# Performance work log

Hardware: AMD Instinct MI355X
Metric: run time of the kernel (lower is better)

Reference implementation:

```python
import jax, jax.numpy as jnp
import numpy as np

N_TOKEN = 267735
CUTOFFS = [20000, 40000, 200000, N_TOKEN]  # includes final n_token
D_EMBED = 1024
D_PROJ = 1024
DIV_VAL = 4
N = 1024  # number of tokens


def setup_inputs() -> dict:
    key = jax.random.key(0)
    ks = jax.random.split(key, 20)
    inp = {}
    inp['hidden'] = jax.random.normal(ks[0], (N, D_PROJ), dtype=jnp.float32)
    inp['target'] = jax.random.randint(ks[1], (N,), 0, N_TOKEN, dtype=jnp.int64)
    cutoff_ends = [0] + CUTOFFS
    # per-cluster params: weight [vocab_i, d_emb_i], bias [vocab_i], proj [d_proj, d_emb_i]
    for i in range(4):
        l, r = cutoff_ends[i], cutoff_ends[i + 1]
        d_i = D_EMBED // (DIV_VAL ** i)
        s = 1.0 / np.sqrt(d_i)
        inp[f'W{i}'] = jax.random.uniform(ks[2 + 3 * i], (r - l, d_i), minval=-s, maxval=s, dtype=jnp.float32)
        inp[f'b{i}'] = jnp.zeros((r - l,), dtype=jnp.float32)
        inp[f'proj{i}'] = jax.random.uniform(ks[3 + 3 * i], (D_PROJ, d_i), minval=-s, maxval=s, dtype=jnp.float32)
    inp['cluster_W'] = jax.random.normal(ks[15], (3, D_EMBED), dtype=jnp.float32) * 0.02
    inp['cluster_b'] = jnp.zeros((3,), dtype=jnp.float32)
    return inp


def _adaptive_nll(hidden, target, W0, b0, proj0, W1, b1, proj1, W2, b2, proj2, W3, b3, proj3, cluster_W, cluster_b):
    cutoff_ends = [0] + CUTOFFS
    # head: shortlist vocab + 3 cluster logits
    head_w = jnp.concatenate([W0, cluster_W], axis=0)          # [20003, d_embed]
    head_b = jnp.concatenate([b0, cluster_b], axis=0)          # [20003]
    head_logit = (hidden @ proj0) @ head_w.T + head_b          # [N, 20003]
    head_lp = jax.nn.log_softmax(head_logit, axis=1)
    # shortlist cluster (i == 0)
    t0 = jnp.clip(target, 0, cutoff_ends[1] - 1)
    lp0 = jnp.take_along_axis(head_lp, t0[:, None], axis=1)[:, 0]
    m0 = target < cutoff_ends[1]
    nll = jnp.where(m0, -lp0, 0.0)
    # tail clusters; faithful to original: head column is head_lp[:, -i]
    tails = [(W1, b1, proj1), (W2, b2, proj2), (W3, b3, proj3)]
    for i, (W_i, b_i, proj_i) in enumerate(tails, start=1):
        l, r = cutoff_ends[i], cutoff_ends[i + 1]
        tail_logit = (hidden @ proj_i) @ W_i.T + b_i           # [N, r-l]
        tail_lp = jax.nn.log_softmax(tail_logit, axis=1)
        ti = jnp.clip(target - l, 0, r - l - 1)
        lp_tail = jnp.take_along_axis(tail_lp, ti[:, None], axis=1)[:, 0]
        lp_i = head_lp[:, -i] + lp_tail
        m_i = (target >= l) & (target < r)
        nll = nll + jnp.where(m_i, -lp_i, 0.0)
    return nll.mean()  # reduction='mean'


def reference(hidden, target, W0, b0, proj0, W1, b1, proj1, W2, b2, proj2, W3, b3, proj3, cluster_W, cluster_b):
    return _adaptive_nll(hidden, target, W0, b0, proj0, W1, b1, proj1, W2, b2, proj2, W3, b3, proj3, cluster_W, cluster_b)
```

## Files before the change

### kernel.cpp

```cpp
#include <hip/hip_runtime.h>
#include <stdint.h>


typedef __attribute__((ext_vector_type(8))) short short8;
typedef __attribute__((ext_vector_type(4))) float f32x4;

__device__ __forceinline__ float bf2f(unsigned short u) {
    union { unsigned int i; float f; } v; v.i = ((unsigned int)u) << 16; return v.f;
}
__device__ __forceinline__ unsigned short f2bf(float f) {
    union { float f; unsigned int i; } v; v.f = f;
    unsigned int u = v.i;
    return (unsigned short)((u + 0x7fffu + ((u >> 16) & 1u)) >> 16);
}
__device__ __forceinline__ float wave_sum(float v) {
    v += __shfl_xor(v, 1, 64);  v += __shfl_xor(v, 2, 64);
    v += __shfl_xor(v, 4, 64);  v += __shfl_xor(v, 8, 64);
    v += __shfl_xor(v, 16, 64); v += __shfl_xor(v, 32, 64);
    return v;
}
__device__ __forceinline__ short8 pack8(float4 a, float4 b) {
    union { int4 i; short8 s; } r;
    r.i.x = __builtin_amdgcn_perm(__float_as_uint(a.y), __float_as_uint(a.x), 0x07060302u);
    r.i.y = __builtin_amdgcn_perm(__float_as_uint(a.w), __float_as_uint(a.z), 0x07060302u);
    r.i.z = __builtin_amdgcn_perm(__float_as_uint(b.y), __float_as_uint(b.x), 0x07060302u);
    r.i.w = __builtin_amdgcn_perm(__float_as_uint(b.w), __float_as_uint(b.z), 0x07060302u);
    return r.s;
}

template <int NK32, int KD>
__device__ __forceinline__ void dev_convw(int bid, const float* __restrict__ W,
                                          unsigned short* __restrict__ Wf,
                                          int vocab, int units) {
    int u = bid * 4 + (threadIdx.x >> 6);
    if (u >= units) return;
    int lane = threadIdx.x & 63, q = lane >> 4, ln = lane & 15;
    int row = u * 16 + ln;
    bool rv = row < vocab;
    const float* src = W + (size_t)row * KD;
#pragma unroll
    for (int ks = 0; ks < NK32; ++ks) {
        int k0 = ks * 32 + q * 8;
        float4 a = {0.f, 0.f, 0.f, 0.f}, b = {0.f, 0.f, 0.f, 0.f};
        if (rv && k0 < KD) {
            a = *(const float4*)(src + k0);
            b = *(const float4*)(src + k0 + 4);
        }
        *(short8*)(Wf + ((size_t)u * NK32 + ks) * 512 + lane * 8) = pack8(a, b);
    }
}

__device__ __forceinline__ void dev_transpose(int bx, int by,
                                              const float* __restrict__ src,
                                              unsigned short* __restrict__ dst,
                                              int K, int N) {
    __shared__ unsigned short tile[32][33];
    int k0 = by * 32, n0 = bx * 32;
    int tx = threadIdx.x & 31, ty = threadIdx.x >> 5;
#pragma unroll
    for (int j = 0; j < 4; ++j) {
        int k = k0 + ty + j * 8, n = n0 + tx;
        float v = (n < N) ? src[(size_t)k * N + n] : 0.f;
        tile[ty + j * 8][tx] = f2bf(v);
    }
    __syncthreads();
#pragma unroll
    for (int j = 0; j < 4; ++j) {
        int n = n0 + ty + j * 8, k = k0 + tx;
        if (n < N) dst[(size_t)n * K + k] = tile[tx][ty + j * 8];
    }
}

__global__ __launch_bounds__(256)
void k_prep(const float* __restrict__ hidden, unsigned short* __restrict__ hid_bf,
            const float* __restrict__ W0, unsigned short* __restrict__ W0f,
            const float* __restrict__ W1, unsigned short* __restrict__ W1f,
            const float* __restrict__ W2, unsigned short* __restrict__ W2f,
            const float* __restrict__ W3, unsigned short* __restrict__ W3f,
            const float* __restrict__ proj0, unsigned short* __restrict__ pT0,
            const float* __restrict__ proj1, unsigned short* __restrict__ pT1,
            const float* __restrict__ proj2, unsigned short* __restrict__ pT2,
            const float* __restrict__ proj3, unsigned short* __restrict__ pT3) {
    int bid = blockIdx.x, tid = threadIdx.x;
    if (bid < 1024) {
        int i = bid * 256 + tid;
        float4 v = ((const float4*)hidden)[i];
        ushort4 o;
        o.x = f2bf(v.x); o.y = f2bf(v.y); o.z = f2bf(v.z); o.w = f2bf(v.w);
        ((ushort4*)hid_bf)[i] = o;
    }
    else if (bid < 1337) dev_convw<32, 1024>(bid - 1024, W0, W0f, 20000, 1250);
    else if (bid < 1650) dev_convw<8,  256> (bid - 1337, W1, W1f, 20000, 1250);
    else if (bid < 4150) dev_convw<2,  64>  (bid - 1650, W2, W2f, 160000, 10000);
    else if (bid < 5209) dev_convw<1,  16>  (bid - 4150, W3, W3f, 67735, 4234);
    else if (bid < 6233) { int i = bid - 5209; dev_transpose(i & 31, i >> 5, proj0, pT0, 1024, 1024); }
    else if (bid < 6489) { int i = bid - 6233; dev_transpose(i & 7,  i >> 3, proj1, pT1, 1024, 256); }
    else if (bid < 6553) { int i = bid - 6489; dev_transpose(i & 1,  i >> 1, proj2, pT2, 1024, 64); }
    else                 { int i = bid - 6553; dev_transpose(0,      i,      proj3, pT3, 1024, 16); }
}

#define BM 128
#define BN 128
#define BK 64
#define LDT 72
template <int NK32O>
__device__ __forceinline__ void dev_gemm(unsigned short* __restrict__ ls,
                                         int bx, int by,
                                         const unsigned short* __restrict__ A, int lda,
                                         const unsigned short* __restrict__ B, int ldb,
                                         unsigned short* __restrict__ Cf,
                                         int N, int K) {
    unsigned short* lsA = ls;
    unsigned short* lsB = ls + BM * LDT;
    int tid = threadIdx.x;
    int mBase = bx * BM, nBase = by * BN;
    int wid = tid >> 6, lane = tid & 63;
    int wr = wid >> 1, wc = wid & 1;
    int q = lane >> 4, ln = lane & 15;
    f32x4 acc[4][4] = {};

    for (int k0 = 0; k0 < K; k0 += BK) {
        __syncthreads();
        int ch = tid & 7;
#pragma unroll
        for (int p = 0; p < 4; ++p) {
            int r = p * 32 + (tid >> 3);
            *(uint4*)(&lsA[r * LDT + ch * 8]) =
                *(const uint4*)(A + (size_t)(mBase + r) * lda + k0 + ch * 8);
        }
#pragma unroll
        for (int p = 0; p < 4; ++p) {
            int r = p * 32 + (tid >> 3);
            uint4 v = {0u, 0u, 0u, 0u};
            if (nBase + r < N)
                v = *(const uint4*)(B + (size_t)(nBase + r) * ldb + k0 + ch * 8);
            *(uint4*)(&lsB[r * LDT + ch * 8]) = v;
        }
        __syncthreads();
#pragma unroll
        for (int ks = 0; ks < 2; ++ks) {
            short8 af[4], bfr[4];
#pragma unroll
            for (int mi = 0; mi < 4; ++mi)
                af[mi] = *(const short8*)(&lsA[(wr * 64 + mi * 16 + ln) * LDT + ks * 32 + q * 8]);
#pragma unroll
            for (int ni = 0; ni < 4; ++ni)
                bfr[ni] = *(const short8*)(&lsB[(wc * 64 + ni * 16 + ln) * LDT + ks * 32 + q * 8]);
#pragma unroll
            for (int mi = 0; mi < 4; ++mi)
#pragma unroll
                for (int ni = 0; ni < 4; ++ni)
                    acc[mi][ni] = __builtin_amdgcn_mfma_f32_16x16x32_bf16(
                        af[mi], bfr[ni], acc[mi][ni], 0, 0, 0);
        }
    }
#pragma unroll
    for (int ni = 0; ni < 4; ++ni) {
        int col = nBase + wc * 64 + ni * 16 + ln;
        if (col < N) {
            int k32 = col >> 5, qc = (col >> 3) & 3, j = col & 7;
#pragma unroll
            for (int mi = 0; mi < 4; ++mi) {
                int m16 = (mBase >> 4) + wr * 4 + mi;
                size_t base = ((size_t)m16 * NK32O + k32) * 512 + (size_t)qc * 128 + j;
#pragma unroll
                for (int r = 0; r < 4; ++r) {
                    int mrem = q * 4 + r;
                    Cf[base + mrem * 8] = f2bf(acc[mi][ni][r]);
                }
            }
        }
    }
}

__global__ __launch_bounds__(256)
void k_gemm_all(const unsigned short* __restrict__ hid_bf,
                const unsigned short* __restrict__ pT0, const unsigned short* __restrict__ pT1,
                const unsigned short* __restrict__ pT2, const unsigned short* __restrict__ pT3,
                unsigned short* __restrict__ h0f, unsigned short* __restrict__ h1f,
                unsigned short* __restrict__ h2f, unsigned short* __restrict__ h3f) {
    __shared__ unsigned short ls[(BM + BN) * LDT];
    int bid = blockIdx.x;
    if (bid < 64)      dev_gemm<32>(ls, bid & 7, bid >> 3, hid_bf, 1024, pT0, 1024, h0f, 1024, 1024);
    else if (bid < 80) { int i = bid - 64; dev_gemm<8>(ls, i & 7, i >> 3, hid_bf, 1024, pT1, 1024, h1f, 256, 1024); }
    else if (bid < 88) dev_gemm<2>(ls, bid - 80, 0, hid_bf, 1024, pT2, 1024, h2f, 64, 1024);
    else               dev_gemm<1>(ls, bid - 88, 0, hid_bf, 1024, pT3, 1024, h3f, 16, 1024);
}

__device__ __forceinline__ void dev_head(int f,
                const unsigned short* __restrict__ Af,
                const unsigned short* __restrict__ Wf,
                const float* __restrict__ bias,
                float* __restrict__ rowsum, int vocab) {
    int u = f & 63;
    int xb = u >> 3;
    int yb = ((f >> 6) << 3) + (u & 7);
    if (yb * 128 >= vocab) return;

    int tid = threadIdx.x, wid = tid >> 6, lane = tid & 63;
    int wr = wid >> 1, wc = wid & 1;
    int q = lane >> 4, ln = lane & 15;
    int mb = xb * 128 + wr * 64;
    int nb = yb * 128 + wc * 64;
    int units = (vocab + 15) >> 4;

    const unsigned short* Ab = Af + (size_t)(mb >> 4) * 32 * 512 + lane * 8;
    const unsigned short* Wp[4];
#pragma unroll
    for (int ni = 0; ni < 4; ++ni)
        Wp[ni] = Wf + (size_t)min((nb >> 4) + ni, units - 1) * 32 * 512 + lane * 8;

    f32x4 acc[4][4] = {};
    short8 Abf[3][4], Wbf[3][4];
    auto LA = [&](short8* d, int kk) {
#pragma unroll
        for (int mi = 0; mi < 4; ++mi)
            d[mi] = *(const short8*)(Ab + ((size_t)mi * 32 + kk) * 512);
    };
    auto LW = [&](short8* d, int kk) {
#pragma unroll
        for (int ni = 0; ni < 4; ++ni)
            d[ni] = *(const short8*)(Wp[ni] + (size_t)kk * 512);
    };
    auto FM = [&](short8* a, short8* w) {
#pragma unroll
        for (int mi = 0; mi < 4; ++mi)
#pragma unroll
            for (int ni = 0; ni < 4; ++ni)
                acc[mi][ni] = __builtin_amdgcn_mfma_f32_16x16x32_bf16(
                    a[mi], w[ni], acc[mi][ni], 0, 0, 0);
    };

    LA(Abf[0], 0); LW(Wbf[0], 0);
    LA(Abf[1], 1); LW(Wbf[1], 1);
#pragma unroll
    for (int ks = 0; ks < 32; ++ks) {
        int nxt = (ks + 2) % 3, cur = ks % 3;
        if (ks + 2 < 32) { LA(Abf[nxt], ks + 2); LW(Wbf[nxt], ks + 2); }
        FM(Abf[cur], Wbf[cur]);
    }

    float s[4][4];
#pragma unroll
    for (int mi = 0; mi < 4; ++mi)
#pragma unroll
        for (int r = 0; r < 4; ++r) s[mi][r] = 0.f;
#pragma unroll
    for (int ni = 0; ni < 4; ++ni) {
        int col = nb + ni * 16 + ln;
        bool valid = col < vocab;
        float b = valid ? bias[col] : 0.f;
#pragma unroll
        for (int mi = 0; mi < 4; ++mi)
#pragma unroll
            for (int r = 0; r < 4; ++r)
                s[mi][r] += valid ? __expf(acc[mi][ni][r] + b) : 0.f;
    }
#pragma unroll
    for (int mi = 0; mi < 4; ++mi)
#pragma unroll
        for (int r = 0; r < 4; ++r) {
            float v = s[mi][r];
            v += __shfl_xor(v, 1, 64);
            v += __shfl_xor(v, 2, 64);
            v += __shfl_xor(v, 4, 64);
            v += __shfl_xor(v, 8, 64);
            s[mi][r] = v;
        }
    int sl = yb & 31;
    if (ln == 0) {
#pragma unroll
        for (int mi = 0; mi < 4; ++mi)
#pragma unroll
            for (int r = 0; r < 4; ++r)
                atomicAdd(&rowsum[sl * 1024 + mb + mi * 16 + q * 4 + r], s[mi][r]);
    }
}

template <int NK32>
__device__ __forceinline__ void dev_tail(int bx, int by,
                const unsigned short* __restrict__ Af,
                const unsigned short* __restrict__ Wf,
                const float* __restrict__ bias,
                float* __restrict__ rowsum,
                int vocab, int units, int ngroups) {
    int tid = threadIdx.x;
    int wid = tid >> 6, lane = tid & 63;
    int q = lane >> 4, ln = lane & 15;
    int m16b = by * 16 + wid * 4;
    int u0 = bx * ngroups;

    short8 af[4][NK32];
#pragma unroll
    for (int mi = 0; mi < 4; ++mi)
#pragma unroll
        for (int ks = 0; ks < NK32; ++ks)
            af[mi][ks] = *(const short8*)(Af + ((size_t)(m16b + mi) * NK32 + ks) * 512 + lane * 8);

    float rs[4][4];
#pragma unroll
    for (int mi = 0; mi < 4; ++mi)
#pragma unroll
        for (int r = 0; r < 4; ++r) rs[mi][r] = 0.f;

    const unsigned short* Wb = Wf + (size_t)lane * 8;
    auto LWG = [&](short8* d, int u) {
        int uc = min(u, units - 1);
#pragma unroll
        for (int ks = 0; ks < NK32; ++ks)
            d[ks] = *(const short8*)(Wb + ((size_t)uc * NK32 + ks) * 512);
    };
    auto CG = [&](short8* w, int u) {
        f32x4 acc[4] = {};
#pragma unroll
        for (int ks = 0; ks < NK32; ++ks)
#pragma unroll
            for (int mi = 0; mi < 4; ++mi)
                acc[mi] = __builtin_amdgcn_mfma_f32_16x16x32_bf16(
                    af[mi][ks], w[ks], acc[mi], 0, 0, 0);
        int col = u * 16 + ln;
        bool valid = col < vocab;
        float b = valid ? bias[col] : 0.f;
#pragma unroll
        for (int mi = 0; mi < 4; ++mi)
#pragma unroll
            for (int r = 0; r < 4; ++r)
                rs[mi][r] += valid ? __expf(acc[mi][r] + b) : 0.f;
    };

    short8 w0[NK32], w1[NK32];
    LWG(w0, u0);
    int g = 0;
    for (; g + 1 < ngroups; g += 2) {
        LWG(w1, u0 + g + 1);
        CG(w0, u0 + g);
        LWG(w0, u0 + g + 2);
        CG(w1, u0 + g + 1);
    }
    if (g < ngroups) CG(w0, u0 + g);

    int sl = bx & 31;
#pragma unroll
    for (int mi = 0; mi < 4; ++mi)
#pragma unroll
        for (int r = 0; r < 4; ++r) {
            float v = rs[mi][r];
            v += __shfl_xor(v, 1, 64);
            v += __shfl_xor(v, 2, 64);
            v += __shfl_xor(v, 4, 64);
            v += __shfl_xor(v, 8, 64);
            if (ln == 0)
                atomicAdd(&rowsum[sl * 1024 + (m16b + mi) * 16 + q * 4 + r], v);
        }
}

__device__ __forceinline__ float frag_dot(const unsigned short* __restrict__ hf,
                                          int NK32, int KdReal, int n,
                                          const float* __restrict__ wrow, int lane) {
    float s = 0.f;
    for (int c = lane; c * 8 < KdReal; c += 64) {
        int k32 = c >> 2, qq = c & 3;
        const unsigned short* p = hf + ((size_t)(n >> 4) * NK32 + k32) * 512 + (qq * 16 + (n & 15)) * 8;
#pragma unroll
        for (int j = 0; j < 8; ++j)
            s += bf2f(p[j]) * wrow[c * 8 + j];
    }
    return wave_sum(s);
}

__device__ __forceinline__ void dev_gather(int bid,
                         const unsigned short* __restrict__ h0f,
                         const unsigned short* __restrict__ h1f,
                         const unsigned short* __restrict__ h2f,
                         const unsigned short* __restrict__ h3f,
                         const float* __restrict__ W0, const float* __restrict__ b0,
                         const float* __restrict__ W1, const float* __restrict__ b1,
                         const float* __restrict__ W2, const float* __restrict__ b2,
                         const float* __restrict__ W3, const float* __restrict__ b3,
                         const float* __restrict__ cW, const float* __restrict__ cb,
                         const int* __restrict__ target,
                         float* __restrict__ rowsum0,
                         float* __restrict__ gat_head,
                         float* __restrict__ gat_tail) {
    int gw = bid * 4 + (threadIdx.x >> 6);
    int lane = threadIdx.x & 63;
    if (gw >= 1024) return;
    int n = gw;
    int t = target[n];

    float cl[3];
#pragma unroll
    for (int j = 0; j < 3; ++j)
        cl[j] = frag_dot(h0f, 32, 1024, n, cW + j * 1024, lane) + cb[j];
    if (lane == 0)
        atomicAdd(&rowsum0[n], __expf(cl[0]) + __expf(cl[1]) + __expf(cl[2]));

    float gh, gt = 0.f;
    if (t < 20000) {
        gh = frag_dot(h0f, 32, 1024, n, W0 + (size_t)t * 1024, lane) + b0[t];
    } else {
        int c, l, Kd, NK32;
        const unsigned short* h; const float* W; const float* b;
        if (t < 40000)       { c = 1; l = 20000;  Kd = 256; NK32 = 8; h = h1f; W = W1; b = b1; }
        else if (t < 200000) { c = 2; l = 40000;  Kd = 64;  NK32 = 2; h = h2f; W = W2; b = b2; }
        else                 { c = 3; l = 200000; Kd = 16;  NK32 = 1; h = h3f; W = W3; b = b3; }
        gh = cl[3 - c];
        gt = frag_dot(h, NK32, Kd, n, W + (size_t)(t - l) * Kd, lane) + b[t - l];
    }
    if (lane == 0) { gat_head[n] = gh; gat_tail[n] = gt; }
}

__global__ __launch_bounds__(256, 2)
void k_logit_all(const unsigned short* __restrict__ h0f, const unsigned short* __restrict__ h1f,
                 const unsigned short* __restrict__ h2f, const unsigned short* __restrict__ h3f,
                 const unsigned short* __restrict__ W0f, const unsigned short* __restrict__ W1f,
                 const unsigned short* __restrict__ W2f, const unsigned short* __restrict__ W3f,
                 const float* __restrict__ W0, const float* __restrict__ b0,
                 const float* __restrict__ W1, const float* __restrict__ b1,
                 const float* __restrict__ W2, const float* __restrict__ b2,
                 const float* __restrict__ W3, const float* __restrict__ b3,
                 const float* __restrict__ cW, const float* __restrict__ cb,
                 const int* __restrict__ target,
                 float* __restrict__ rowsum,
                 float* __restrict__ gat_head, float* __restrict__ gat_tail) {
    int bid = blockIdx.x;
    if (bid < 1280) {
        dev_head(bid, h0f, W0f, b0, rowsum, 20000);
    } else if (bid < 1536) {
        int i = bid - 1280;
        dev_tail<8>(i & 63, i >> 6, h1f, W1f, b1, rowsum + 32768, 20000, 1250, 20);
    } else if (bid < 2176) {
        int i = bid - 1536;
        dev_tail<2>(i % 160, i / 160, h2f, W2f, b2, rowsum + 65536, 160000, 10000, 63);
    } else if (bid < 2688) {
        int i = bid - 2176;
        dev_tail<1>(i & 127, i >> 7, h3f, W3f, b3, rowsum + 98304, 67735, 4234, 34);
    } else {
        dev_gather(bid - 2688, h0f, h1f, h2f, h3f, W0, b0, W1, b1, W2, b2, W3, b3,
                   cW, cb, target, rowsum, gat_head, gat_tail);
    }
}

__global__ void k_finalize(const float* __restrict__ rs,
                           const float* __restrict__ gat_head,
                           const float* __restrict__ gat_tail,
                           const int* __restrict__ target,
                           float* __restrict__ out) {
    __shared__ float red[16];
    int n = threadIdx.x;
    int t = target[n];
    float r0 = 0.f;
#pragma unroll
    for (int s = 0; s < 32; ++s) r0 += rs[s * 1024 + n];
    float nll = __logf(r0) - gat_head[n];
    int c = (t < 20000) ? 0 : (t < 40000) ? 1 : (t < 200000) ? 2 : 3;
    if (c > 0) {
        float rc = 0.f;
#pragma unroll
        for (int s = 0; s < 32; ++s) rc += rs[c * 32768 + s * 1024 + n];
        nll += __logf(rc) - gat_tail[n];
    }
    float sm = wave_sum(nll);
    int wid = n >> 6, lane = n & 63;
    if (lane == 0) red[wid] = sm;
    __syncthreads();
    if (n == 0) {
        float tot = 0.f;
#pragma unroll
        for (int i = 0; i < 16; ++i) tot += red[i];
        out[0] = tot / 1024.0f;
    }
}

extern "C" void kernel_launch(void* const* d_in, const int* in_sizes, int n_in,
                              void* d_out, int out_size, void* d_ws, size_t ws_size,
                              hipStream_t stream) {
    const float* hidden = (const float*)d_in[0];
    const int*   target = (const int*)d_in[1];
    const float* W0 = (const float*)d_in[2];
    const float* b0 = (const float*)d_in[3];
    const float* proj0 = (const float*)d_in[4];
    const float* W1 = (const float*)d_in[5];
    const float* b1 = (const float*)d_in[6];
    const float* proj1 = (const float*)d_in[7];
    const float* W2 = (const float*)d_in[8];
    const float* b2 = (const float*)d_in[9];
    const float* proj2 = (const float*)d_in[10];
    const float* W3 = (const float*)d_in[11];
    const float* b3 = (const float*)d_in[12];
    const float* proj3 = (const float*)d_in[13];
    const float* cW = (const float*)d_in[14];
    const float* cb = (const float*)d_in[15];

    char* ws = (char*)d_ws;
    unsigned short* hid_bf = (unsigned short*)(ws + 0x000000);
    unsigned short* pT0 = (unsigned short*)(ws + 0x200000);
    unsigned short* pT1 = (unsigned short*)(ws + 0x400000);
    unsigned short* pT2 = (unsigned short*)(ws + 0x480000);
    unsigned short* pT3 = (unsigned short*)(ws + 0x4A0000);
    unsigned short* h0f = (unsigned short*)(ws + 0x4A8000);
    unsigned short* h1f = (unsigned short*)(ws + 0x6A8000);
    unsigned short* h2f = (unsigned short*)(ws + 0x728000);
    unsigned short* h3f = (unsigned short*)(ws + 0x748000);
    float* rowsum   = (float*)(ws + 0x758000);
    float* gat_head = (float*)(ws + 0x7D8000);
    float* gat_tail = (float*)(ws + 0x7D9000);
    unsigned short* W0f = (unsigned short*)(ws + 0x00800000);
    unsigned short* W1f = (unsigned short*)(ws + 0x02F10000);
    unsigned short* W2f = (unsigned short*)(ws + 0x038D4000);
    unsigned short* W3f = (unsigned short*)(ws + 0x04C5C000);

    hipMemsetAsync(ws + 0x748000, 0, 0x92000, stream);

    k_prep<<<6585, 256, 0, stream>>>(hidden, hid_bf, W0, W0f, W1, W1f, W2, W2f, W3, W3f,
                                     proj0, pT0, proj1, pT1, proj2, pT2, proj3, pT3);

    k_gemm_all<<<96, 256, 0, stream>>>(hid_bf, pT0, pT1, pT2, pT3, h0f, h1f, h2f, h3f);

    k_logit_all<<<2944, 256, 0, stream>>>(h0f, h1f, h2f, h3f, W0f, W1f, W2f, W3f,
                                          W0, b0, W1, b1, W2, b2, W3, b3,
                                          cW, cb, target, rowsum, gat_head, gat_tail);

    k_finalize<<<1, 1024, 0, stream>>>(rowsum, gat_head, gat_tail, target, (float*)d_out);
}
```

Measured before the change: 412.8 us.

## Overlap weight conversion with projection GEMMs and pad biases to drop bounds checks

Moves the large fp32-to-bf16 weight repacking out of the prep kernel and into the same launch as the projection GEMMs, so the few GEMM blocks run alongside the bandwidth-bound conversion. Biases are copied into padded buffers filled with -1e30 so the logit kernels can drop per-column validity checks and clamped unit indices. The head-style tiled streaming kernel is templated and reused for cluster 1 in place of the tail kernel, and its software pipeline uses two buffers instead of three. This adds extra workspace and a bias-fill pass, and changes how work is split across the GPU for the middle cluster.

```diff
diff --git a/kernel.cpp b/kernel.cpp
--- a/kernel.cpp
+++ b/kernel.cpp
@@ -28,28 +28,6 @@
     return r.s;
 }
 
-template <int NK32, int KD>
-__device__ __forceinline__ void dev_convw(int bid, const float* __restrict__ W,
-                                          unsigned short* __restrict__ Wf,
-                                          int vocab, int units) {
-    int u = bid * 4 + (threadIdx.x >> 6);
-    if (u >= units) return;
-    int lane = threadIdx.x & 63, q = lane >> 4, ln = lane & 15;
-    int row = u * 16 + ln;
-    bool rv = row < vocab;
-    const float* src = W + (size_t)row * KD;
-#pragma unroll
-    for (int ks = 0; ks < NK32; ++ks) {
-        int k0 = ks * 32 + q * 8;
-        float4 a = {0.f, 0.f, 0.f, 0.f}, b = {0.f, 0.f, 0.f, 0.f};
-        if (rv && k0 < KD) {
-            a = *(const float4*)(src + k0);
-            b = *(const float4*)(src + k0 + 4);
-        }
-        *(short8*)(Wf + ((size_t)u * NK32 + ks) * 512 + lane * 8) = pack8(a, b);
-    }
-}
-
 __device__ __forceinline__ void dev_transpose(int bx, int by,
                                               const float* __restrict__ src,
                                               unsigned short* __restrict__ dst,
@@ -71,16 +49,22 @@
     }
 }
 
+__device__ __forceinline__ void dev_biasfill(int bid, const float* __restrict__ b,
+                                             float* __restrict__ bp, int vocab, int padded) {
+    int i = bid * 256 + threadIdx.x;
+    if (i < padded) bp[i] = (i < vocab) ? b[i] : -1e30f;
+}
+
 __global__ __launch_bounds__(256)
-void k_prep(const float* __restrict__ hidden, unsigned short* __restrict__ hid_bf,
-            const float* __restrict__ W0, unsigned short* __restrict__ W0f,
-            const float* __restrict__ W1, unsigned short* __restrict__ W1f,
-            const float* __restrict__ W2, unsigned short* __restrict__ W2f,
-            const float* __restrict__ W3, unsigned short* __restrict__ W3f,
-            const float* __restrict__ proj0, unsigned short* __restrict__ pT0,
-            const float* __restrict__ proj1, unsigned short* __restrict__ pT1,
-            const float* __restrict__ proj2, unsigned short* __restrict__ pT2,
-            const float* __restrict__ proj3, unsigned short* __restrict__ pT3) {
+void k_pre(const float* __restrict__ hidden, unsigned short* __restrict__ hid_bf,
+           const float* __restrict__ proj0, unsigned short* __restrict__ pT0,
+           const float* __restrict__ proj1, unsigned short* __restrict__ pT1,
+           const float* __restrict__ proj2, unsigned short* __restrict__ pT2,
+           const float* __restrict__ proj3, unsigned short* __restrict__ pT3,
+           const float* __restrict__ b0, float* __restrict__ b0p,
+           const float* __restrict__ b1, float* __restrict__ b1p,
+           const float* __restrict__ b2, float* __restrict__ b2p,
+           const float* __restrict__ b3, float* __restrict__ b3p) {
     int bid = blockIdx.x, tid = threadIdx.x;
     if (bid < 1024) {
         int i = bid * 256 + tid;
@@ -89,14 +73,36 @@
         o.x = f2bf(v.x); o.y = f2bf(v.y); o.z = f2bf(v.z); o.w = f2bf(v.w);
         ((ushort4*)hid_bf)[i] = o;
     }
-    else if (bid < 1337) dev_convw<32, 1024>(bid - 1024, W0, W0f, 20000, 1250);
-    else if (bid < 1650) dev_convw<8,  256> (bid - 1337, W1, W1f, 20000, 1250);
-    else if (bid < 4150) dev_convw<2,  64>  (bid - 1650, W2, W2f, 160000, 10000);
-    else if (bid < 5209) dev_convw<1,  16>  (bid - 4150, W3, W3f, 67735, 4234);
-    else if (bid < 6233) { int i = bid - 5209; dev_transpose(i & 31, i >> 5, proj0, pT0, 1024, 1024); }
-    else if (bid < 6489) { int i = bid - 6233; dev_transpose(i & 7,  i >> 3, proj1, pT1, 1024, 256); }
-    else if (bid < 6553) { int i = bid - 6489; dev_transpose(i & 1,  i >> 1, proj2, pT2, 1024, 64); }
-    else                 { int i = bid - 6553; dev_transpose(0,      i,      proj3, pT3, 1024, 16); }
+    else if (bid < 2048) { int i = bid - 1024; dev_transpose(i & 31, i >> 5, proj0, pT0, 1024, 1024); }
+    else if (bid < 2304) { int i = bid - 2048; dev_transpose(i & 7,  i >> 3, proj1, pT1, 1024, 256); }
+    else if (bid < 2368) { int i = bid - 2304; dev_transpose(i & 1,  i >> 1, proj2, pT2, 1024, 64); }
+    else if (bid < 2400) { int i = bid - 2368; dev_transpose(0,      i,      proj3, pT3, 1024, 16); }
+    else if (bid < 2479) dev_biasfill(bid - 2400, b0, b0p, 20000, 20096);
+    else if (bid < 2558) dev_biasfill(bid - 2479, b1, b1p, 20000, 20096);
+    else if (bid < 3188) dev_biasfill(bid - 2558, b2, b2p, 160000, 161280);
+    else                 dev_biasfill(bid - 3188, b3, b3p, 67735, 69632);
+}
+
+template <int NK32, int KD>
+__device__ __forceinline__ void dev_convw(int bid, const float* __restrict__ W,
+                                          unsigned short* __restrict__ Wf,
+                                          int vocab, int upad) {
+    int u = bid * 4 + (threadIdx.x >> 6);
+    if (u >= upad) return;
+    int lane = threadIdx.x & 63, q = lane >> 4, ln = lane & 15;
+    int row = u * 16 + ln;
+    bool rv = row < vocab;
+    const float* src = W + (size_t)row * KD;
+#pragma unroll
+    for (int ks = 0; ks < NK32; ++ks) {
+        int k0 = ks * 32 + q * 8;
+        float4 a = {0.f, 0.f, 0.f, 0.f}, b = {0.f, 0.f, 0.f, 0.f};
+        if (rv && k0 < KD) {
+            a = *(const float4*)(src + k0);
+            b = *(const float4*)(src + k0 + 4);
+        }
+        *(short8*)(Wf + ((size_t)u * NK32 + ks) * 512 + lane * 8) = pack8(a, b);
+    }
 }
 
 #define BM 128
@@ -174,48 +180,56 @@
 }
 
 __global__ __launch_bounds__(256)
-void k_gemm_all(const unsigned short* __restrict__ hid_bf,
-                const unsigned short* __restrict__ pT0, const unsigned short* __restrict__ pT1,
-                const unsigned short* __restrict__ pT2, const unsigned short* __restrict__ pT3,
-                unsigned short* __restrict__ h0f, unsigned short* __restrict__ h1f,
-                unsigned short* __restrict__ h2f, unsigned short* __restrict__ h3f) {
+void k_mid(const unsigned short* __restrict__ hid_bf,
+           const unsigned short* __restrict__ pT0, const unsigned short* __restrict__ pT1,
+           const unsigned short* __restrict__ pT2, const unsigned short* __restrict__ pT3,
+           unsigned short* __restrict__ h0f, unsigned short* __restrict__ h1f,
+           unsigned short* __restrict__ h2f, unsigned short* __restrict__ h3f,
+           const float* __restrict__ W0, unsigned short* __restrict__ W0f,
+           const float* __restrict__ W1, unsigned short* __restrict__ W1f,
+           const float* __restrict__ W2, unsigned short* __restrict__ W2f,
+           const float* __restrict__ W3, unsigned short* __restrict__ W3f) {
     __shared__ unsigned short ls[(BM + BN) * LDT];
     int bid = blockIdx.x;
-    if (bid < 64)      dev_gemm<32>(ls, bid & 7, bid >> 3, hid_bf, 1024, pT0, 1024, h0f, 1024, 1024);
-    else if (bid < 80) { int i = bid - 64; dev_gemm<8>(ls, i & 7, i >> 3, hid_bf, 1024, pT1, 1024, h1f, 256, 1024); }
-    else if (bid < 88) dev_gemm<2>(ls, bid - 80, 0, hid_bf, 1024, pT2, 1024, h2f, 64, 1024);
-    else               dev_gemm<1>(ls, bid - 88, 0, hid_bf, 1024, pT3, 1024, h3f, 16, 1024);
-}
-
-__device__ __forceinline__ void dev_head(int f,
+    if (bid < 64)        dev_gemm<32>(ls, bid & 7, bid >> 3, hid_bf, 1024, pT0, 1024, h0f, 1024, 1024);
+    else if (bid < 80)   { int i = bid - 64; dev_gemm<8>(ls, i & 7, i >> 3, hid_bf, 1024, pT1, 1024, h1f, 256, 1024); }
+    else if (bid < 88)   dev_gemm<2>(ls, bid - 80, 0, hid_bf, 1024, pT2, 1024, h2f, 64, 1024);
+    else if (bid < 96)   dev_gemm<1>(ls, bid - 88, 0, hid_bf, 1024, pT3, 1024, h3f, 16, 1024);
+    else if (bid < 410)  dev_convw<32, 1024>(bid - 96,   W0, W0f, 20000, 1256);
+    else if (bid < 724)  dev_convw<8,  256> (bid - 410,  W1, W1f, 20000, 1256);
+    else if (bid < 3244) dev_convw<2,  64>  (bid - 724,  W2, W2f, 160000, 10080);
+    else                 dev_convw<1,  16>  (bid - 3244, W3, W3f, 67735, 4352);
+}
+
+template <int NK32>
+__device__ __forceinline__ void dev_stream(int f,
                 const unsigned short* __restrict__ Af,
                 const unsigned short* __restrict__ Wf,
-                const float* __restrict__ bias,
-                float* __restrict__ rowsum, int vocab) {
+                const float* __restrict__ biasp,
+                float* __restrict__ rowsum) {
     int u = f & 63;
     int xb = u >> 3;
     int yb = ((f >> 6) << 3) + (u & 7);
-    if (yb * 128 >= vocab) return;
+    if (yb >= 157) return;
 
     int tid = threadIdx.x, wid = tid >> 6, lane = tid & 63;
     int wr = wid >> 1, wc = wid & 1;
     int q = lane >> 4, ln = lane & 15;
     int mb = xb * 128 + wr * 64;
     int nb = yb * 128 + wc * 64;
-    int units = (vocab + 15) >> 4;
-
-    const unsigned short* Ab = Af + (size_t)(mb >> 4) * 32 * 512 + lane * 8;
+
+    const unsigned short* Ab = Af + (size_t)(mb >> 4) * NK32 * 512 + lane * 8;
     const unsigned short* Wp[4];
 #pragma unroll
     for (int ni = 0; ni < 4; ++ni)
-        Wp[ni] = Wf + (size_t)min((nb >> 4) + ni, units - 1) * 32 * 512 + lane * 8;
+        Wp[ni] = Wf + (size_t)((nb >> 4) + ni) * NK32 * 512 + lane * 8;
 
     f32x4 acc[4][4] = {};
-    short8 Abf[3][4], Wbf[3][4];
+    short8 a0[4], a1[4], w0[4], w1[4];
     auto LA = [&](short8* d, int kk) {
 #pragma unroll
         for (int mi = 0; mi < 4; ++mi)
-            d[mi] = *(const short8*)(Ab + ((size_t)mi * 32 + kk) * 512);
+            d[mi] = *(const short8*)(Ab + ((size_t)mi * NK32 + kk) * 512);
     };
     auto LW = [&](short8* d, int kk) {
 #pragma unroll
@@ -231,13 +245,13 @@
                     a[mi], w[ni], acc[mi][ni], 0, 0, 0);
     };
 
-    LA(Abf[0], 0); LW(Wbf[0], 0);
-    LA(Abf[1], 1); LW(Wbf[1], 1);
-#pragma unroll
-    for (int ks = 0; ks < 32; ++ks) {
-        int nxt = (ks + 2) % 3, cur = ks % 3;
-        if (ks + 2 < 32) { LA(Abf[nxt], ks + 2); LW(Wbf[nxt], ks + 2); }
-        FM(Abf[cur], Wbf[cur]);
+    LA(a0, 0); LW(w0, 0);
+#pragma unroll
+    for (int ks = 0; ks < NK32; ks += 2) {
+        LA(a1, ks + 1); LW(w1, ks + 1);
+        FM(a0, w0);
+        if (ks + 2 < NK32) { LA(a0, ks + 2); LW(w0, ks + 2); }
+        FM(a1, w1);
     }
 
     float s[4][4];
@@ -247,14 +261,12 @@
         for (int r = 0; r < 4; ++r) s[mi][r] = 0.f;
 #pragma unroll
     for (int ni = 0; ni < 4; ++ni) {
-        int col = nb + ni * 16 + ln;
-        bool valid = col < vocab;
-        float b = valid ? bias[col] : 0.f;
+        float b = biasp[nb + ni * 16 + ln];
 #pragma unroll
         for (int mi = 0; mi < 4; ++mi)
 #pragma unroll
             for (int r = 0; r < 4; ++r)
-                s[mi][r] += valid ? __expf(acc[mi][ni][r] + b) : 0.f;
+                s[mi][r] += __expf(acc[mi][ni][r] + b);
     }
 #pragma unroll
     for (int mi = 0; mi < 4; ++mi)
@@ -281,9 +293,8 @@
 __device__ __forceinline__ void dev_tail(int bx, int by,
                 const unsigned short* __restrict__ Af,
                 const unsigned short* __restrict__ Wf,
-                const float* __restrict__ bias,
-                float* __restrict__ rowsum,
-                int vocab, int units, int ngroups) {
+                const float* __restrict__ biasp,
+                float* __restrict__ rowsum, int ngroups) {
     int tid = threadIdx.x;
     int wid = tid >> 6, lane = tid & 63;
     int q = lane >> 4, ln = lane & 15;
@@ -305,10 +316,9 @@
 
     const unsigned short* Wb = Wf + (size_t)lane * 8;
     auto LWG = [&](short8* d, int u) {
-        int uc = min(u, units - 1);
 #pragma unroll
         for (int ks = 0; ks < NK32; ++ks)
-            d[ks] = *(const short8*)(Wb + ((size_t)uc * NK32 + ks) * 512);
+            d[ks] = *(const short8*)(Wb + ((size_t)u * NK32 + ks) * 512);
     };
     auto CG = [&](short8* w, int u) {
         f32x4 acc[4] = {};
@@ -318,14 +328,12 @@
             for (int mi = 0; mi < 4; ++mi)
                 acc[mi] = __builtin_amdgcn_mfma_f32_16x16x32_bf16(
                     af[mi][ks], w[ks], acc[mi], 0, 0, 0);
-        int col = u * 16 + ln;
-        bool valid = col < vocab;
-        float b = valid ? bias[col] : 0.f;
+        float b = biasp[u * 16 + ln];
 #pragma unroll
         for (int mi = 0; mi < 4; ++mi)
 #pragma unroll
             for (int r = 0; r < 4; ++r)
-                rs[mi][r] += valid ? __expf(acc[mi][r] + b) : 0.f;
+                rs[mi][r] += __expf(acc[mi][r] + b);
     };
 
     short8 w0[NK32], w1[NK32];
@@ -415,6 +423,8 @@
                  const unsigned short* __restrict__ h2f, const unsigned short* __restrict__ h3f,
                  const unsigned short* __restrict__ W0f, const unsigned short* __restrict__ W1f,
                  const unsigned short* __restrict__ W2f, const unsigned short* __restrict__ W3f,
+                 const float* __restrict__ b0p, const float* __restrict__ b1p,
+                 const float* __restrict__ b2p, const float* __restrict__ b3p,
                  const float* __restrict__ W0, const float* __restrict__ b0,
                  const float* __restrict__ W1, const float* __restrict__ b1,
                  const float* __restrict__ W2, const float* __restrict__ b2,
@@ -425,18 +435,17 @@
                  float* __restrict__ gat_head, float* __restrict__ gat_tail) {
     int bid = blockIdx.x;
     if (bid < 1280) {
-        dev_head(bid, h0f, W0f, b0, rowsum, 20000);
-    } else if (bid < 1536) {
-        int i = bid - 1280;
-        dev_tail<8>(i & 63, i >> 6, h1f, W1f, b1, rowsum + 32768, 20000, 1250, 20);
-    } else if (bid < 2176) {
-        int i = bid - 1536;
-        dev_tail<2>(i % 160, i / 160, h2f, W2f, b2, rowsum + 65536, 160000, 10000, 63);
-    } else if (bid < 2688) {
-        int i = bid - 2176;
-        dev_tail<1>(i & 127, i >> 7, h3f, W3f, b3, rowsum + 98304, 67735, 4234, 34);
+        dev_stream<32>(bid, h0f, W0f, b0p, rowsum);
+    } else if (bid < 2560) {
+        dev_stream<8>(bid - 1280, h1f, W1f, b1p, rowsum + 32768);
+    } else if (bid < 3200) {
+        int i = bid - 2560;
+        dev_tail<2>(i % 160, i / 160, h2f, W2f, b2p, rowsum + 65536, 63);
+    } else if (bid < 3712) {
+        int i = bid - 3200;
+        dev_tail<1>(i & 127, i >> 7, h3f, W3f, b3p, rowsum + 98304, 34);
     } else {
-        dev_gather(bid - 2688, h0f, h1f, h2f, h3f, W0, b0, W1, b1, W2, b2, W3, b3,
+        dev_gather(bid - 3712, h0f, h1f, h2f, h3f, W0, b0, W1, b1, W2, b2, W3, b3,
                    cW, cb, target, rowsum, gat_head, gat_tail);
     }
 }
@@ -506,18 +515,25 @@
     float* gat_head = (float*)(ws + 0x7D8000);
     float* gat_tail = (float*)(ws + 0x7D9000);
     unsigned short* W0f = (unsigned short*)(ws + 0x00800000);
-    unsigned short* W1f = (unsigned short*)(ws + 0x02F10000);
-    unsigned short* W2f = (unsigned short*)(ws + 0x038D4000);
-    unsigned short* W3f = (unsigned short*)(ws + 0x04C5C000);
+    unsigned short* W1f = (unsigned short*)(ws + 0x02F40000);
+    unsigned short* W2f = (unsigned short*)(ws + 0x03910000);
+    unsigned short* W3f = (unsigned short*)(ws + 0x04CC0000);
+    float* b0p = (float*)(ws + 0x05100000);
+    float* b1p = (float*)(ws + 0x05114000);
+    float* b2p = (float*)(ws + 0x05128000);
+    float* b3p = (float*)(ws + 0x051C8000);
 
     hipMemsetAsync(ws + 0x748000, 0, 0x92000, stream);
 
-    k_prep<<<6585, 256, 0, stream>>>(hidden, hid_bf, W0, W0f, W1, W1f, W2, W2f, W3, W3f,
-                                     proj0, pT0, proj1, pT1, proj2, pT2, proj3, pT3);
-
-    k_gemm_all<<<96, 256, 0, stream>>>(hid_bf, pT0, pT1, pT2, pT3, h0f, h1f, h2f, h3f);
-
-    k_logit_all<<<2944, 256, 0, stream>>>(h0f, h1f, h2f, h3f, W0f, W1f, W2f, W3f,
+    k_pre<<<3460, 256, 0, stream>>>(hidden, hid_bf,
+                                    proj0, pT0, proj1, pT1, proj2, pT2, proj3, pT3,
+                                    b0, b0p, b1, b1p, b2, b2p, b3, b3p);
+
+    k_mid<<<4332, 256, 0, stream>>>(hid_bf, pT0, pT1, pT2, pT3, h0f, h1f, h2f, h3f,
+                                    W0, W0f, W1, W1f, W2, W2f, W3, W3f);
+
+    k_logit_all<<<3968, 256, 0, stream>>>(h0f, h1f, h2f, h3f, W0f, W1f, W2f, W3f,
+                                          b0p, b1p, b2p, b3p,
                                           W0, b0, W1, b1, W2, b2, W3, b3,
                                           cW, cb, target, rowsum, gat_head, gat_tail);
 
```

New measurement: 395.4 us. 4.2% less time.
